# Performance work log

Hardware: AMD Instinct MI355X
Metric: run time of the kernel (lower is better)

## Reference

```python
import jax, jax.numpy as jnp
import numpy as np

H = 768
L = 9
M = 5            # max_span_length
CTX_RATIO = 0.5
NEG_INF = -1e30


def setup_inputs() -> dict:
    key = jax.random.key(0)
    ks = jax.random.split(key, 12)
    B, S = 4, 2048
    sc = 1.0 / np.sqrt(H)
    return {
        "sequence_output": jax.random.normal(ks[0], (B, S, H), dtype=jnp.float32),
        "Wc": jax.random.normal(ks[1], (H, L), dtype=jnp.float32) * sc,
        "bc": jnp.zeros((L,), dtype=jnp.float32),
        "wa": jax.random.normal(ks[2], (H,), dtype=jnp.float32) * sc,
        "ba": jnp.zeros((), dtype=jnp.float32),
        "W1": jax.random.normal(ks[3], (2 * H, H), dtype=jnp.float32) * (1.0 / np.sqrt(2 * H)),
        "b1": jnp.zeros((H,), dtype=jnp.float32),
        "gamma": jnp.ones((H,), dtype=jnp.float32),
        "beta": jnp.zeros((H,), dtype=jnp.float32),
        "W2": jax.random.normal(ks[4], (H, L), dtype=jnp.float32) * sc,
        "b2": jnp.zeros((L,), dtype=jnp.float32),
    }


def reference(sequence_output, Wc, bc, wa, ba, W1, b1, gamma, beta, W2, b2):
    x = sequence_output                        # [B,S,H]
    B, S, _ = x.shape
    base_logits = jnp.einsum('bsh,hl->bsl', x, Wc) + bc   # [B,S,L]

    # sliding-window indices: window [i-M, i+M] clipped to [0, S)
    offsets = jnp.arange(-M, M + 1)            # [W]
    idx = jnp.arange(S)[:, None] + offsets     # [S,W]
    valid = (idx >= 0) & (idx < S)             # [S,W]
    idx_c = jnp.clip(idx, 0, S - 1)            # [S,W]

    # attention scores over window (span_attention linear -> scalar per token)
    scores = jnp.einsum('bsh,h->bs', x, wa) + ba           # [B,S]
    win_scores = scores[:, idx_c]                          # [B,S,W]
    win_scores = jnp.where(valid[None], win_scores, NEG_INF)
    attn = jax.nn.softmax(win_scores, axis=-1)             # [B,S,W]

    win_tokens = x[:, idx_c]                               # [B,S,W,H] gather
    weighted_ctx = jnp.einsum('bsw,bswh->bsh', attn, win_tokens)

    token_with_ctx = jnp.concatenate([x, weighted_ctx], axis=-1)  # [B,S,2H]
    h = jnp.einsum('bsd,dh->bsh', token_with_ctx, W1) + b1
    # LayerNorm (eps = 1e-5, torch default)
    mu = jnp.mean(h, axis=-1, keepdims=True)
    var = jnp.mean((h - mu) ** 2, axis=-1, keepdims=True)
    h = (h - mu) * jax.lax.rsqrt(var + 1e-5) * gamma + beta
    h = jax.nn.gelu(h, approximate=False)                  # torch nn.GELU default (erf)
    ctx_logits = jnp.einsum('bsh,hl->bsl', h, W2) + b2

    return (1.0 - CTX_RATIO) * base_logits + CTX_RATIO * ctx_logits
```

## Files before the change

### kernel.cpp

```cpp
#include <hip/hip_runtime.h>
#include <hip/hip_bf16.h>
#include <math.h>

#define S_LEN 2048
#define BATCH 4
#define HDIM 768
#define LOUT 9
#define NROWS (BATCH*S_LEN)
#define K2H 1536
#define WIN 11
#define NEG_INF_F (-1e30f)

typedef __attribute__((ext_vector_type(4))) float f32x4;
typedef __attribute__((ext_vector_type(8))) short bf16x8;

static __device__ __forceinline__ void async_ld16(const void* g, void* l) {
  __builtin_amdgcn_global_load_lds((const __attribute__((address_space(1))) void*)g,
                                   (__attribute__((address_space(3))) void*)l, 16, 0, 0);
}

static __device__ __forceinline__ unsigned short f2bf(float f) {
  union { float f; unsigned int u; } v; v.f = f;
  unsigned int u = v.u;
  unsigned int r = (u + 0x7fffu + ((u >> 16) & 1u)) >> 16;
  return (unsigned short)r;
}

static __device__ __forceinline__ float bf2f(unsigned short h) {
  union { unsigned int u; float f; } v; v.u = ((unsigned int)h) << 16;
  return v.f;
}

__global__ __launch_bounds__(256) void k_prep_w1t(const float* __restrict__ W1,
                                                  unsigned short* __restrict__ W1t) {
  __shared__ float tile[32][33];
  int bk = blockIdx.x % 48;
  int bn = blockIdx.x / 48;
  int tc = threadIdx.x % 32;
  int tr = threadIdx.x / 32;
  #pragma unroll
  for (int i = 0; i < 32; i += 8) {
    tile[tr + i][tc] = W1[(bk*32 + tr + i) * HDIM + bn*32 + tc];
  }
  __syncthreads();
  #pragma unroll
  for (int i = 0; i < 32; i += 8) {
    W1t[(bn*32 + tr + i) * K2H + bk*32 + tc] = f2bf(tile[tc][tr + i]);
  }
}

__global__ __launch_bounds__(192) void k_prep(const float* __restrict__ x,
                                              const float* __restrict__ wa,
                                              const float* __restrict__ ba,
                                              const float* __restrict__ Wc,
                                              const float* __restrict__ bc,
                                              unsigned short* __restrict__ xc,
                                              float* __restrict__ scores,
                                              float* __restrict__ base) {
  __shared__ float red[3][LOUT + 1];
  int bid = blockIdx.x;
  int row = (bid & 7) * 1024 + (bid >> 3);
  int t = threadIdx.x;
  int lane = t & 63, wave = t >> 6;
  const float4 v = *(const float4*)(x + row * HDIM + t * 4);
  const float4 w = *(const float4*)(wa + t * 4);
  ushort4 o;
  o.x = f2bf(v.x); o.y = f2bf(v.y); o.z = f2bf(v.z); o.w = f2bf(v.w);
  *(ushort4*)(xc + row * K2H + t * 4) = o;

  float pv[LOUT + 1];
  pv[LOUT] = v.x * w.x + v.y * w.y + v.z * w.z + v.w * w.w;
  #pragma unroll
  for (int l = 0; l < LOUT; ++l) pv[l] = 0.f;
  const float xvv[4] = { v.x, v.y, v.z, v.w };
  #pragma unroll
  for (int j = 0; j < 4; ++j) {
    const float* wr = Wc + (t * 4 + j) * LOUT;
    #pragma unroll
    for (int l = 0; l < LOUT; ++l) pv[l] += xvv[j] * wr[l];
  }
  #pragma unroll
  for (int l = 0; l <= LOUT; ++l)
    #pragma unroll
    for (int m = 1; m < 64; m <<= 1) pv[l] += __shfl_xor(pv[l], m);
  if (lane == 0) {
    #pragma unroll
    for (int l = 0; l <= LOUT; ++l) red[wave][l] = pv[l];
  }
  __syncthreads();
  if (t < LOUT) {
    base[row * LOUT + t] = red[0][t] + red[1][t] + red[2][t] + bc[t];
  } else if (t == LOUT) {
    scores[row] = red[0][LOUT] + red[1][LOUT] + red[2][LOUT] + ba[0];
  }
}

__global__ __launch_bounds__(192) void k_ctx(const float* __restrict__ scores,
                                             unsigned short* __restrict__ xc) {
  __shared__ float swin[WIN];
  int bid = blockIdx.x;
  int row = (bid & 7) * 1024 + (bid >> 3);
  int b = row >> 11, s = row & 2047;
  int t = threadIdx.x;
  if (t < WIN) {
    int j = s - 5 + t;
    bool valid = (j >= 0) && (j < S_LEN);
    int jc = valid ? j : (j < 0 ? 0 : S_LEN - 1);
    swin[t] = valid ? scores[b * S_LEN + jc] : NEG_INF_F;
  }
  __syncthreads();
  float mx = swin[0];
  #pragma unroll
  for (int w = 1; w < WIN; ++w) mx = fmaxf(mx, swin[w]);
  float es[WIN], ssum = 0.f;
  #pragma unroll
  for (int w = 0; w < WIN; ++w) {
    float sv = swin[w];
    es[w] = (sv > -1e29f) ? __expf(sv - mx) : 0.f;
    ssum += es[w];
  }
  float inv = 1.f / ssum;
  float c0 = 0.f, c1 = 0.f, c2 = 0.f, c3 = 0.f;
  #pragma unroll
  for (int w = 0; w < WIN; ++w) {
    float aw = es[w] * inv;
    int j = s - 5 + w;
    int jc = (j < 0) ? 0 : ((j >= S_LEN) ? S_LEN - 1 : j);
    const ushort4 uv = *(const ushort4*)(xc + (((long)b * S_LEN + jc) * K2H) + t * 4);
    c0 += aw * bf2f(uv.x);
    c1 += aw * bf2f(uv.y);
    c2 += aw * bf2f(uv.z);
    c3 += aw * bf2f(uv.w);
  }
  ushort4 o;
  o.x = f2bf(c0); o.y = f2bf(c1); o.z = f2bf(c2); o.w = f2bf(c3);
  *(ushort4*)(xc + row * K2H + HDIM + t * 4) = o;
}

__global__ __launch_bounds__(256, 3) void k_gemm(const unsigned short* __restrict__ A,
                                                 const unsigned short* __restrict__ Bt,
                                                 const float* __restrict__ b1,
                                                 float* __restrict__ Hout) {
  __shared__ unsigned short As[4][128 * 32];
  __shared__ unsigned short Bs[4][64 * 32];
  int bid = blockIdx.x;
  int obid = (bid & 7) * 96 + (bid >> 3);
  int bm = obid / 12, bn = obid % 12;
  int t = threadIdx.x;
  int lane = t & 63, wave = t >> 6;

  int fl = ((lane >> 2) ^ (lane >> 4)) & 3;
  int sSrc = ((lane & 3) ^ fl);
  int rIn = lane >> 2;

  const unsigned short* gA = A  + (bm * 128 + wave * 32 + rIn) * K2H + sSrc * 8;
  const unsigned short* gB = Bt + (bn * 64  + wave * 16 + rIn) * K2H + sSrc * 8;

  f32x4 acc[2][4] = {};

  int laneRow = lane & 15;
  int slot = lane >> 4;
  int fr = ((lane & 3) ^ ((lane >> 2) & 3));
  int rdOff = ((slot ^ fr) & 3) * 8;

#define STAGE(buf, kt) do {                                                    \
    async_ld16(gA + (kt),             &As[buf][(wave * 32) * 32]);             \
    async_ld16(gA + 16 * K2H + (kt),  &As[buf][(wave * 32 + 16) * 32]);        \
    async_ld16(gB + (kt),             &Bs[buf][(wave * 16) * 32]);             \
  } while (0)

#define COMPUTE(buf) do {                                                      \
    bf16x8 af[2], bfv[4];                                                      \
    _Pragma("unroll")                                                          \
    for (int m = 0; m < 2; ++m)                                                \
      af[m] = *(const bf16x8*)(&As[buf][(wave * 32 + m * 16 + laneRow) * 32 + rdOff]); \
    _Pragma("unroll")                                                          \
    for (int n = 0; n < 4; ++n)                                                \
      bfv[n] = *(const bf16x8*)(&Bs[buf][(n * 16 + laneRow) * 32 + rdOff]);    \
    __builtin_amdgcn_s_setprio(1);                                             \
    _Pragma("unroll")                                                          \
    for (int m = 0; m < 2; ++m)                                                \
      _Pragma("unroll")                                                        \
      for (int n = 0; n < 4; ++n)                                              \
        acc[m][n] = __builtin_amdgcn_mfma_f32_16x16x32_bf16(af[m], bfv[n], acc[m][n], 0, 0, 0); \
    __builtin_amdgcn_s_setprio(0);                                             \
  } while (0)

#define WBAR(n) asm volatile("s_waitcnt vmcnt(" #n ")\n\ts_barrier" ::: "memory")

  STAGE(0, 0);
  STAGE(1, 32);
  STAGE(2, 64);

  for (int tt = 0; tt < 45; ++tt) {
    WBAR(6);
    STAGE((tt + 3) & 3, (tt + 3) * 32);
    COMPUTE(tt & 3);
  }
  WBAR(6);  COMPUTE(1);
  WBAR(3);  COMPUTE(2);
  WBAR(0);  COMPUTE(3);

  int orow = bm * 128 + wave * 32 + (lane >> 4) * 4;
  int ocol = bn * 64 + (lane & 15);
  #pragma unroll
  for (int m = 0; m < 2; ++m)
    #pragma unroll
    for (int n = 0; n < 4; ++n) {
      int col = ocol + n * 16;
      float bv = b1[col];
      #pragma unroll
      for (int r = 0; r < 4; ++r) {
        Hout[(orow + m * 16 + r) * HDIM + col] = acc[m][n][r] + bv;
      }
    }
#undef STAGE
#undef COMPUTE
#undef WBAR
}

__global__ __launch_bounds__(192) void k_ln(const float* __restrict__ Hin,
                                            const float* __restrict__ gamma,
                                            const float* __restrict__ beta,
                                            const float* __restrict__ W2,
                                            const float* __restrict__ b2,
                                            const float* __restrict__ base,
                                            float* __restrict__ out) {
  __shared__ float redS[3], redQ[3], redp[3][LOUT];
  int row = blockIdx.x;
  int t = threadIdx.x;
  int lane = t & 63, wave = t >> 6;
  const float4 v = *(const float4*)(Hin + row * HDIM + t * 4);
  float s1 = v.x + v.y + v.z + v.w;
  float s2 = v.x*v.x + v.y*v.y + v.z*v.z + v.w*v.w;
  #pragma unroll
  for (int m = 1; m < 64; m <<= 1) { s1 += __shfl_xor(s1, m); s2 += __shfl_xor(s2, m); }
  if (lane == 0) { redS[wave] = s1; redQ[wave] = s2; }
  __syncthreads();
  s1 = redS[0] + redS[1] + redS[2];
  s2 = redQ[0] + redQ[1] + redQ[2];
  float mu = s1 * (1.f / HDIM);
  float var = s2 * (1.f / HDIM) - mu * mu;
  float rstd = rsqrtf(var + 1e-5f);
  const float4 g4 = *(const float4*)(gamma + t * 4);
  const float4 be4 = *(const float4*)(beta + t * 4);
  float p[LOUT] = {};
  const float vv[4] = { v.x, v.y, v.z, v.w };
  const float gv[4] = { g4.x, g4.y, g4.z, g4.w };
  const float bv[4] = { be4.x, be4.y, be4.z, be4.w };
  #pragma unroll
  for (int j = 0; j < 4; ++j) {
    float g = (vv[j] - mu) * rstd * gv[j] + bv[j];
    float gg = 0.5f * g * (1.f + erff(g * 0.70710678118654752f));
    const float* wrow = W2 + (t * 4 + j) * LOUT;
    #pragma unroll
    for (int l = 0; l < LOUT; ++l) p[l] += gg * wrow[l];
  }
  #pragma unroll
  for (int l = 0; l < LOUT; ++l)
    #pragma unroll
    for (int m = 1; m < 64; m <<= 1) p[l] += __shfl_xor(p[l], m);
  if (lane == 0) {
    #pragma unroll
    for (int l = 0; l < LOUT; ++l) redp[wave][l] = p[l];
  }
  __syncthreads();
  if (t < LOUT) {
    float cl = redp[0][t] + redp[1][t] + redp[2][t] + b2[t];
    out[row * LOUT + t] = 0.5f * base[row * LOUT + t] + 0.5f * cl;
  }
}

extern "C" void kernel_launch(void* const* d_in, const int* in_sizes, int n_in,
                              void* d_out, int out_size, void* d_ws, size_t ws_size,
                              hipStream_t stream) {
  const float* x     = (const float*)d_in[0];
  const float* Wc    = (const float*)d_in[1];
  const float* bc    = (const float*)d_in[2];
  const float* wa    = (const float*)d_in[3];
  const float* ba    = (const float*)d_in[4];
  const float* W1    = (const float*)d_in[5];
  const float* b1    = (const float*)d_in[6];
  const float* gamma = (const float*)d_in[7];
  const float* beta  = (const float*)d_in[8];
  const float* W2    = (const float*)d_in[9];
  const float* b2    = (const float*)d_in[10];
  float* out = (float*)d_out;

  char* ws = (char*)d_ws;
  unsigned short* xc  = (unsigned short*)(ws);
  unsigned short* w1t = (unsigned short*)(ws + 25165824);
  float* scores       = (float*)(ws + 27525120);
  float* base         = (float*)(ws + 27557888);
  float* hbuf         = (float*)(ws + 27852800);

  k_prep_w1t<<<dim3(1152), dim3(256), 0, stream>>>(W1, w1t);
  k_prep    <<<dim3(8192), dim3(192), 0, stream>>>(x, wa, ba, Wc, bc, xc, scores, base);
  k_ctx     <<<dim3(8192), dim3(192), 0, stream>>>(scores, xc);
  k_gemm    <<<dim3(768),  dim3(256), 0, stream>>>(xc, w1t, b1, hbuf);
  k_ln      <<<dim3(8192), dim3(192), 0, stream>>>(hbuf, gamma, beta, W2, b2, base, out);
}
```

Baseline: 179.2 us.

## Deepen GEMM K-tile to 64 with triple buffering and store hidden in bf16

The W1 GEMM now stages 64-wide K tiles instead of 32, using three LDS buffers with an 8-way XOR swizzle in place of four 32-wide buffers, which halves the number of barrier/stage iterations. Occupancy drops from 3 to 2 blocks per CU and the setprio hints are removed. The GEMM output hidden buffer is also written as bf16 instead of fp32, and the LayerNorm kernel reads bf16, halving that intermediate's memory traffic. The cost is some LayerNorm-input precision and a larger LDS footprint per block.

```diff
diff --git a/kernel.cpp b/kernel.cpp
--- a/kernel.cpp
+++ b/kernel.cpp
@@ -137,69 +137,90 @@
   *(ushort4*)(xc + row * K2H + HDIM + t * 4) = o;
 }
 
-__global__ __launch_bounds__(256, 3) void k_gemm(const unsigned short* __restrict__ A,
+__global__ __launch_bounds__(256, 2) void k_gemm(const unsigned short* __restrict__ A,
                                                  const unsigned short* __restrict__ Bt,
                                                  const float* __restrict__ b1,
-                                                 float* __restrict__ Hout) {
-  __shared__ unsigned short As[4][128 * 32];
-  __shared__ unsigned short Bs[4][64 * 32];
+                                                 unsigned short* __restrict__ Hout) {
+  __shared__ unsigned short As[3][128 * 64];
+  __shared__ unsigned short Bs[3][64 * 64];
   int bid = blockIdx.x;
   int obid = (bid & 7) * 96 + (bid >> 3);
   int bm = obid / 12, bn = obid % 12;
   int t = threadIdx.x;
   int lane = t & 63, wave = t >> 6;
 
-  int fl = ((lane >> 2) ^ (lane >> 4)) & 3;
-  int sSrc = ((lane & 3) ^ fl);
-  int rIn = lane >> 2;
-
-  const unsigned short* gA = A  + (bm * 128 + wave * 32 + rIn) * K2H + sSrc * 8;
-  const unsigned short* gB = Bt + (bn * 64  + wave * 16 + rIn) * K2H + sSrc * 8;
+  int rowc = lane >> 3;
+  int slot = lane & 7;
+  const unsigned short* gAj[4];
+  #pragma unroll
+  for (int j = 0; j < 4; ++j) {
+    int rloc = j * 32 + wave * 8 + rowc;
+    int f = (rloc ^ (rloc >> 3)) & 7;
+    gAj[j] = A + (bm * 128 + rloc) * K2H + ((slot ^ f) & 7) * 8;
+  }
+  const unsigned short* gBj[2];
+  #pragma unroll
+  for (int j = 0; j < 2; ++j) {
+    int rloc = j * 32 + wave * 8 + rowc;
+    int f = (rloc ^ (rloc >> 3)) & 7;
+    gBj[j] = Bt + (bn * 64 + rloc) * K2H + ((slot ^ f) & 7) * 8;
+  }
 
   f32x4 acc[2][4] = {};
 
-  int laneRow = lane & 15;
-  int slot = lane >> 4;
-  int fr = ((lane & 3) ^ ((lane >> 2) & 3));
-  int rdOff = ((slot ^ fr) & 3) * 8;
-
 #define STAGE(buf, kt) do {                                                    \
-    async_ld16(gA + (kt),             &As[buf][(wave * 32) * 32]);             \
-    async_ld16(gA + 16 * K2H + (kt),  &As[buf][(wave * 32 + 16) * 32]);        \
-    async_ld16(gB + (kt),             &Bs[buf][(wave * 16) * 32]);             \
+    _Pragma("unroll")                                                          \
+    for (int j = 0; j < 4; ++j)                                                \
+      async_ld16(gAj[j] + (kt), &As[buf][(j * 32 + wave * 8) * 64]);           \
+    _Pragma("unroll")                                                          \
+    for (int j = 0; j < 2; ++j)                                                \
+      async_ld16(gBj[j] + (kt), &Bs[buf][(j * 32 + wave * 8) * 64]);           \
   } while (0)
 
 #define COMPUTE(buf) do {                                                      \
-    bf16x8 af[2], bfv[4];                                                      \
+    const unsigned short* aB = &As[buf][0];                                    \
+    const unsigned short* bB = &Bs[buf][0];                                    \
     _Pragma("unroll")                                                          \
-    for (int m = 0; m < 2; ++m)                                                \
-      af[m] = *(const bf16x8*)(&As[buf][(wave * 32 + m * 16 + laneRow) * 32 + rdOff]); \
-    _Pragma("unroll")                                                          \
-    for (int n = 0; n < 4; ++n)                                                \
-      bfv[n] = *(const bf16x8*)(&Bs[buf][(n * 16 + laneRow) * 32 + rdOff]);    \
-    __builtin_amdgcn_s_setprio(1);                                             \
-    _Pragma("unroll")                                                          \
-    for (int m = 0; m < 2; ++m)                                                \
+    for (int kk = 0; kk < 2; ++kk) {                                           \
+      bf16x8 af[2], bfv[4];                                                    \
       _Pragma("unroll")                                                        \
-      for (int n = 0; n < 4; ++n)                                              \
-        acc[m][n] = __builtin_amdgcn_mfma_f32_16x16x32_bf16(af[m], bfv[n], acc[m][n], 0, 0, 0); \
-    __builtin_amdgcn_s_setprio(0);                                             \
+      for (int m = 0; m < 2; ++m) {                                            \
+        int rl = wave * 32 + m * 16 + (lane & 15);                             \
+        int f = (rl ^ (rl >> 3)) & 7;                                          \
+        int sl = (kk * 4 + (lane >> 4)) ^ f;                                   \
+        af[m] = *(const bf16x8*)(aB + rl * 64 + sl * 8);                       \
+      }                                                                        \
+      _Pragma("unroll")                                                        \
+      for (int n = 0; n < 4; ++n) {                                            \
+        int rl = n * 16 + (lane & 15);                                         \
+        int f = (rl ^ (rl >> 3)) & 7;                                          \
+        int sl = (kk * 4 + (lane >> 4)) ^ f;                                   \
+        bfv[n] = *(const bf16x8*)(bB + rl * 64 + sl * 8);                      \
+      }                                                                        \
+      _Pragma("unroll")                                                        \
+      for (int m = 0; m < 2; ++m)                                              \
+        _Pragma("unroll")                                                      \
+        for (int n = 0; n < 4; ++n)                                            \
+          acc[m][n] = __builtin_amdgcn_mfma_f32_16x16x32_bf16(af[m], bfv[n], acc[m][n], 0, 0, 0); \
+    }                                                                          \
   } while (0)
 
 #define WBAR(n) asm volatile("s_waitcnt vmcnt(" #n ")\n\ts_barrier" ::: "memory")
 
   STAGE(0, 0);
-  STAGE(1, 32);
-  STAGE(2, 64);
-
-  for (int tt = 0; tt < 45; ++tt) {
+  STAGE(1, 64);
+
+  int bufc = 0;
+  for (int tt = 0; tt < 22; ++tt) {
     WBAR(6);
-    STAGE((tt + 3) & 3, (tt + 3) * 32);
-    COMPUTE(tt & 3);
-  }
-  WBAR(6);  COMPUTE(1);
-  WBAR(3);  COMPUTE(2);
-  WBAR(0);  COMPUTE(3);
+    int bufn = bufc + 2; if (bufn >= 3) bufn -= 3;
+    STAGE(bufn, (tt + 2) * 64);
+    COMPUTE(bufc);
+    bufc = (bufc == 2) ? 0 : bufc + 1;
+  }
+  WBAR(6);  COMPUTE(bufc);
+  bufc = (bufc == 2) ? 0 : bufc + 1;
+  WBAR(0);  COMPUTE(bufc);
 
   int orow = bm * 128 + wave * 32 + (lane >> 4) * 4;
   int ocol = bn * 64 + (lane & 15);
@@ -211,7 +232,7 @@
       float bv = b1[col];
       #pragma unroll
       for (int r = 0; r < 4; ++r) {
-        Hout[(orow + m * 16 + r) * HDIM + col] = acc[m][n][r] + bv;
+        Hout[(orow + m * 16 + r) * HDIM + col] = f2bf(acc[m][n][r] + bv);
       }
     }
 #undef STAGE
@@ -219,7 +240,7 @@
 #undef WBAR
 }
 
-__global__ __launch_bounds__(192) void k_ln(const float* __restrict__ Hin,
+__global__ __launch_bounds__(192) void k_ln(const unsigned short* __restrict__ Hin,
                                             const float* __restrict__ gamma,
                                             const float* __restrict__ beta,
                                             const float* __restrict__ W2,
@@ -230,9 +251,10 @@
   int row = blockIdx.x;
   int t = threadIdx.x;
   int lane = t & 63, wave = t >> 6;
-  const float4 v = *(const float4*)(Hin + row * HDIM + t * 4);
-  float s1 = v.x + v.y + v.z + v.w;
-  float s2 = v.x*v.x + v.y*v.y + v.z*v.z + v.w*v.w;
+  const ushort4 hv = *(const ushort4*)(Hin + row * HDIM + t * 4);
+  const float vv[4] = { bf2f(hv.x), bf2f(hv.y), bf2f(hv.z), bf2f(hv.w) };
+  float s1 = vv[0] + vv[1] + vv[2] + vv[3];
+  float s2 = vv[0]*vv[0] + vv[1]*vv[1] + vv[2]*vv[2] + vv[3]*vv[3];
   #pragma unroll
   for (int m = 1; m < 64; m <<= 1) { s1 += __shfl_xor(s1, m); s2 += __shfl_xor(s2, m); }
   if (lane == 0) { redS[wave] = s1; redQ[wave] = s2; }
@@ -244,10 +266,9 @@
   float rstd = rsqrtf(var + 1e-5f);
   const float4 g4 = *(const float4*)(gamma + t * 4);
   const float4 be4 = *(const float4*)(beta + t * 4);
-  float p[LOUT] = {};
-  const float vv[4] = { v.x, v.y, v.z, v.w };
   const float gv[4] = { g4.x, g4.y, g4.z, g4.w };
   const float bv[4] = { be4.x, be4.y, be4.z, be4.w };
+  float p[LOUT] = {};
   #pragma unroll
   for (int j = 0; j < 4; ++j) {
     float g = (vv[j] - mu) * rstd * gv[j] + bv[j];
@@ -292,7 +313,7 @@
   unsigned short* w1t = (unsigned short*)(ws + 25165824);
   float* scores       = (float*)(ws + 27525120);
   float* base         = (float*)(ws + 27557888);
-  float* hbuf         = (float*)(ws + 27852800);
+  unsigned short* hbuf = (unsigned short*)(ws + 27852800);
 
   k_prep_w1t<<<dim3(1152), dim3(256), 0, stream>>>(W1, w1t);
   k_prep    <<<dim3(8192), dim3(192), 0, stream>>>(x, wa, ba, Wc, bc, xc, scores, base);
```

Result: slower. 187.8 us (+4.8%).

## Split-K GEMM with 128x128 tiles and reduce partials in LayerNorm kernel

Applied to the files above, without the earlier changes.

The W1 GEMM now uses 128x128 output tiles with a 2x2 wave layout and 4x4 MFMA fragments per wave. It splits K into two halves so the grid stays at 768 blocks. Each half writes a separate fp32 partial buffer, and the LayerNorm kernel adds both partials plus the bias. This raises arithmetic intensity per LDS load. The cost is an extra fp32 H-sized write and read, plus a shallower double-buffered pipeline with full __syncthreads instead of the previous 4-stage vmcnt-based pipeline.

```diff
diff --git a/kernel.cpp b/kernel.cpp
--- a/kernel.cpp
+++ b/kernel.cpp
@@ -8,6 +8,7 @@
 #define LOUT 9
 #define NROWS (BATCH*S_LEN)
 #define K2H 1536
+#define KHALF 768
 #define WIN 11
 #define NEG_INF_F (-1e30f)
 
@@ -139,87 +140,85 @@
 
 __global__ __launch_bounds__(256, 3) void k_gemm(const unsigned short* __restrict__ A,
                                                  const unsigned short* __restrict__ Bt,
-                                                 const float* __restrict__ b1,
                                                  float* __restrict__ Hout) {
-  __shared__ unsigned short As[4][128 * 32];
-  __shared__ unsigned short Bs[4][64 * 32];
+  __shared__ unsigned short As[2][128 * 32];
+  __shared__ unsigned short Bs[2][128 * 32];
   int bid = blockIdx.x;
   int obid = (bid & 7) * 96 + (bid >> 3);
-  int bm = obid / 12, bn = obid % 12;
+  int kh = obid / 384;
+  int mt = obid % 384;
+  int bm = mt / 6, bn = mt % 6;
   int t = threadIdx.x;
   int lane = t & 63, wave = t >> 6;
-
-  int fl = ((lane >> 2) ^ (lane >> 4)) & 3;
-  int sSrc = ((lane & 3) ^ fl);
-  int rIn = lane >> 2;
-
-  const unsigned short* gA = A  + (bm * 128 + wave * 32 + rIn) * K2H + sSrc * 8;
-  const unsigned short* gB = Bt + (bn * 64  + wave * 16 + rIn) * K2H + sSrc * 8;
-
-  f32x4 acc[2][4] = {};
-
-  int laneRow = lane & 15;
-  int slot = lane >> 4;
-  int fr = ((lane & 3) ^ ((lane >> 2) & 3));
-  int rdOff = ((slot ^ fr) & 3) * 8;
+  int wm = wave >> 1, wn = wave & 1;
+
+  int rowc = lane >> 2;
+  int fST = ((lane >> 2) ^ (lane >> 4)) & 3;
+  int sST = (lane & 3) ^ fST;
+  const unsigned short* gA0 = A  + (long)(bm * 128 + wave * 16 + rowc) * K2H + kh * KHALF + sST * 8;
+  const unsigned short* gB0 = Bt + (long)(bn * 128 + wave * 16 + rowc) * K2H + kh * KHALF + sST * 8;
+
+  int fR = ((lane & 3) ^ ((lane >> 2) & 3)) & 3;
+  int slR = ((lane >> 4) ^ fR) & 3;
+  int arow = wm * 64 + (lane & 15);
+  int brow = wn * 64 + (lane & 15);
+
+  f32x4 acc[4][4] = {};
 
 #define STAGE(buf, kt) do {                                                    \
-    async_ld16(gA + (kt),             &As[buf][(wave * 32) * 32]);             \
-    async_ld16(gA + 16 * K2H + (kt),  &As[buf][(wave * 32 + 16) * 32]);        \
-    async_ld16(gB + (kt),             &Bs[buf][(wave * 16) * 32]);             \
+    async_ld16(gA0 + (kt),            &As[buf][(wave * 16) * 32]);             \
+    async_ld16(gA0 + 64 * K2H + (kt), &As[buf][(64 + wave * 16) * 32]);        \
+    async_ld16(gB0 + (kt),            &Bs[buf][(wave * 16) * 32]);             \
+    async_ld16(gB0 + 64 * K2H + (kt), &Bs[buf][(64 + wave * 16) * 32]);        \
   } while (0)
 
 #define COMPUTE(buf) do {                                                      \
-    bf16x8 af[2], bfv[4];                                                      \
+    bf16x8 af[4], bfv[4];                                                      \
     _Pragma("unroll")                                                          \
-    for (int m = 0; m < 2; ++m)                                                \
-      af[m] = *(const bf16x8*)(&As[buf][(wave * 32 + m * 16 + laneRow) * 32 + rdOff]); \
+    for (int m = 0; m < 4; ++m)                                                \
+      af[m] = *(const bf16x8*)(&As[buf][(arow + m * 16) * 32 + slR * 8]);      \
     _Pragma("unroll")                                                          \
     for (int n = 0; n < 4; ++n)                                                \
-      bfv[n] = *(const bf16x8*)(&Bs[buf][(n * 16 + laneRow) * 32 + rdOff]);    \
-    __builtin_amdgcn_s_setprio(1);                                             \
+      bfv[n] = *(const bf16x8*)(&Bs[buf][(brow + n * 16) * 32 + slR * 8]);     \
     _Pragma("unroll")                                                          \
-    for (int m = 0; m < 2; ++m)                                                \
+    for (int m = 0; m < 4; ++m)                                                \
       _Pragma("unroll")                                                        \
       for (int n = 0; n < 4; ++n)                                              \
         acc[m][n] = __builtin_amdgcn_mfma_f32_16x16x32_bf16(af[m], bfv[n], acc[m][n], 0, 0, 0); \
-    __builtin_amdgcn_s_setprio(0);                                             \
   } while (0)
 
-#define WBAR(n) asm volatile("s_waitcnt vmcnt(" #n ")\n\ts_barrier" ::: "memory")
-
   STAGE(0, 0);
-  STAGE(1, 32);
-  STAGE(2, 64);
-
-  for (int tt = 0; tt < 45; ++tt) {
-    WBAR(6);
-    STAGE((tt + 3) & 3, (tt + 3) * 32);
-    COMPUTE(tt & 3);
-  }
-  WBAR(6);  COMPUTE(1);
-  WBAR(3);  COMPUTE(2);
-  WBAR(0);  COMPUTE(3);
-
-  int orow = bm * 128 + wave * 32 + (lane >> 4) * 4;
-  int ocol = bn * 64 + (lane & 15);
-  #pragma unroll
-  for (int m = 0; m < 2; ++m)
+  __syncthreads();
+  int cur = 0;
+  #pragma unroll 1
+  for (int tt = 0; tt < 23; ++tt) {
+    STAGE(cur ^ 1, (tt + 1) * 32);
+    COMPUTE(cur);
+    __syncthreads();
+    cur ^= 1;
+  }
+  COMPUTE(cur);
+
+  float* Hp = Hout + (long)kh * NROWS * HDIM;
+  int orow = bm * 128 + wm * 64 + (lane >> 4) * 4;
+  int ocol = bn * 128 + wn * 64 + (lane & 15);
+  #pragma unroll
+  for (int m = 0; m < 4; ++m)
     #pragma unroll
     for (int n = 0; n < 4; ++n) {
       int col = ocol + n * 16;
-      float bv = b1[col];
       #pragma unroll
       for (int r = 0; r < 4; ++r) {
-        Hout[(orow + m * 16 + r) * HDIM + col] = acc[m][n][r] + bv;
+        Hp[(long)(orow + m * 16 + r) * HDIM + col] = acc[m][n][r];
       }
     }
 #undef STAGE
 #undef COMPUTE
-#undef WBAR
-}
-
-__global__ __launch_bounds__(192) void k_ln(const float* __restrict__ Hin,
+}
+
+__global__ __launch_bounds__(192) void k_ln(const float* __restrict__ H0,
+                                            const float* __restrict__ H1,
+                                            const float* __restrict__ b1,
                                             const float* __restrict__ gamma,
                                             const float* __restrict__ beta,
                                             const float* __restrict__ W2,
@@ -230,9 +229,13 @@
   int row = blockIdx.x;
   int t = threadIdx.x;
   int lane = t & 63, wave = t >> 6;
-  const float4 v = *(const float4*)(Hin + row * HDIM + t * 4);
-  float s1 = v.x + v.y + v.z + v.w;
-  float s2 = v.x*v.x + v.y*v.y + v.z*v.z + v.w*v.w;
+  const float4 p0 = *(const float4*)(H0 + (long)row * HDIM + t * 4);
+  const float4 p1 = *(const float4*)(H1 + (long)row * HDIM + t * 4);
+  const float4 b14 = *(const float4*)(b1 + t * 4);
+  const float vv[4] = { p0.x + p1.x + b14.x, p0.y + p1.y + b14.y,
+                        p0.z + p1.z + b14.z, p0.w + p1.w + b14.w };
+  float s1 = vv[0] + vv[1] + vv[2] + vv[3];
+  float s2 = vv[0]*vv[0] + vv[1]*vv[1] + vv[2]*vv[2] + vv[3]*vv[3];
   #pragma unroll
   for (int m = 1; m < 64; m <<= 1) { s1 += __shfl_xor(s1, m); s2 += __shfl_xor(s2, m); }
   if (lane == 0) { redS[wave] = s1; redQ[wave] = s2; }
@@ -244,10 +247,9 @@
   float rstd = rsqrtf(var + 1e-5f);
   const float4 g4 = *(const float4*)(gamma + t * 4);
   const float4 be4 = *(const float4*)(beta + t * 4);
-  float p[LOUT] = {};
-  const float vv[4] = { v.x, v.y, v.z, v.w };
   const float gv[4] = { g4.x, g4.y, g4.z, g4.w };
   const float bv[4] = { be4.x, be4.y, be4.z, be4.w };
+  float p[LOUT] = {};
   #pragma unroll
   for (int j = 0; j < 4; ++j) {
     float g = (vv[j] - mu) * rstd * gv[j] + bv[j];
@@ -297,6 +299,7 @@
   k_prep_w1t<<<dim3(1152), dim3(256), 0, stream>>>(W1, w1t);
   k_prep    <<<dim3(8192), dim3(192), 0, stream>>>(x, wa, ba, Wc, bc, xc, scores, base);
   k_ctx     <<<dim3(8192), dim3(192), 0, stream>>>(scores, xc);
-  k_gemm    <<<dim3(768),  dim3(256), 0, stream>>>(xc, w1t, b1, hbuf);
-  k_ln      <<<dim3(8192), dim3(192), 0, stream>>>(hbuf, gamma, beta, W2, b2, base, out);
-}
+  k_gemm    <<<dim3(768),  dim3(256), 0, stream>>>(xc, w1t, hbuf);
+  k_ln      <<<dim3(8192), dim3(192), 0, stream>>>(hbuf, hbuf + (long)NROWS * HDIM, b1,
+                                                   gamma, beta, W2, b2, base, out);
+}
```

Measured after the change: 174.7 us. -2.5%, faster.
